# Optimization experiments

Measured on AMD Instinct MI355X. Metric: run time of the kernel, lower is better.

Reference implementation:

```python
import jax, jax.numpy as jnp
import numpy as np
from jax import lax

B, CIN, COUT, K, H, W = 16, 256, 256, 3, 128, 128
R = 16  # LoRA rank


def setup_inputs() -> dict:
    key = jax.random.key(0)
    ks = jax.random.split(key, 16)
    s = 0.05
    return {
        "x": jax.random.normal(ks[0], (B, CIN, H, W), jnp.float32),
        "wms": jax.random.normal(ks[1], (2, B, 32), jnp.float32),
        "conv_w": jax.random.normal(ks[2], (COUT, CIN, K, K), jnp.float32) * s,
        "conv_b": jax.random.normal(ks[3], (COUT,), jnp.float32) * s,
        "e1_w1": jax.random.normal(ks[4], (128, 32), jnp.float32) * s,
        "e1_b1": jax.random.normal(ks[5], (128,), jnp.float32) * s,
        "e1_w2": jax.random.normal(ks[6], (256, 128), jnp.float32) * s,
        "e1_b2": jax.random.normal(ks[7], (256,), jnp.float32) * s,
        "e2_w1": jax.random.normal(ks[8], (128, 32), jnp.float32) * s,
        "e2_b1": jax.random.normal(ks[9], (128,), jnp.float32) * s,
        "e2_w2": jax.random.normal(ks[10], (256, 128), jnp.float32) * s,
        "e2_b2": jax.random.normal(ks[11], (256,), jnp.float32) * s,
        "lora_A1": jax.random.normal(ks[12], (R, CIN * K), jnp.float32),
        "lora_A2": jax.random.normal(ks[13], (R, CIN * K), jnp.float32),
        "lora_B": jax.random.normal(ks[14], (COUT * K, R), jnp.float32) * s,
    }


def _embed(v, w1, b1, w2, b2):
    # Linear(32,128) -> LeakyReLU(0.2) -> Linear(128,256)
    h = v @ w1.T + b1
    h = jnp.where(h >= 0, h, 0.2 * h)
    return h @ w2.T + b2


def _conv_same(x, w):
    # NCHW conv, stride 1, padding 1
    return lax.conv_general_dilated(x, w, (1, 1), [(1, 1), (1, 1)],
                                    dimension_numbers=("NCHW", "OIHW", "NCHW"))


def reference(x, wms, conv_w, conv_b, e1_w1, e1_b1, e1_w2, e1_b2,
              e2_w1, e2_b1, e2_w2, e2_b2, lora_A1, lora_A2, lora_B):
    wm1, wm2 = wms[0], wms[1]
    coff1 = _embed(wm1, e1_w1, e1_b1, e1_w2, e1_b2).reshape(B, R, R)
    coff2 = _embed(wm2, e2_w1, e2_b1, e2_w2, e2_b2).reshape(B, R, R)

    org = _conv_same(x, conv_w) + conv_b[None, :, None, None]

    # per-sample LoRA weights: (COUT*K, R) @ (R,R) @ (R, CIN*K) -> (B, COUT, CIN, K, K)
    wA = jnp.einsum('pr,brq,qc->bpc', lora_B, coff1, lora_A1).reshape(B, COUT, CIN, K, K)
    wB = jnp.einsum('pr,brq,qc->bpc', lora_B, coff2, lora_A2).reshape(B, COUT, CIN, K, K)

    def per_sample_conv(xi, wi):
        return _conv_same(xi[None], wi)[0]

    outA = jax.vmap(per_sample_conv)(x, wA)
    outB = jax.vmap(per_sample_conv)(x, wB)
    return org + outA + outB
```

## Files before the change

### kernel.cpp

```cpp
#include <hip/hip_runtime.h>
#include <hip/hip_bf16.h>
#include <stdint.h>

typedef __bf16 bf16x8 __attribute__((ext_vector_type(8)));
typedef float f32x4 __attribute__((ext_vector_type(4)));
typedef unsigned short ushort8v __attribute__((ext_vector_type(8)));

#define NB    16
#define CIN   256
#define COUT  256
#define HH    128
#define WW    128

#define OFF_ZROW  0u
#define OFF_COFF  (1u << 16)
#define OFF_TMPS  (1u << 17)
#define OFF_WEFF  (1u << 20)
#define OFF_XT    (20u * 1024u * 1024u)
#define XT_PER_B  (128u * 128u * 256u * 2u)

__device__ inline void gload16(const void* g, void* l) {
  __builtin_amdgcn_global_load_lds(
      (const __attribute__((address_space(1))) void*)g,
      (__attribute__((address_space(3))) void*)l, 16, 0, 0);
}

__device__ inline ushort f2bf(float f) {
  __hip_bfloat16 h = __float2bfloat16(f);
  union { __hip_bfloat16 b; ushort u; } cv;
  cv.b = h;
  return cv.u;
}

__global__ void k_coff(const float* __restrict__ wms,
                       const float* __restrict__ w1a, const float* __restrict__ b1a,
                       const float* __restrict__ w2a, const float* __restrict__ b2a,
                       const float* __restrict__ w1b, const float* __restrict__ b1b,
                       const float* __restrict__ w2b, const float* __restrict__ b2b,
                       float* __restrict__ coff) {
  int br = blockIdx.x >> 4, b = blockIdx.x & 15;
  const float* w1 = br ? w1b : w1a;
  const float* b1 = br ? b1b : b1a;
  const float* w2 = br ? w2b : w2a;
  const float* b2 = br ? b2b : b2a;
  const float* v = wms + (br * 16 + b) * 32;
  __shared__ float h[128];
  int t = threadIdx.x;
  if (t < 128) {
    float a = b1[t];
#pragma unroll
    for (int i = 0; i < 32; ++i) a += w1[t * 32 + i] * v[i];
    h[t] = a >= 0.f ? a : 0.2f * a;
  }
  __syncthreads();
  float a = b2[t];
  for (int j = 0; j < 128; ++j) a += w2[t * 128 + j] * h[j];
  coff[(br * 16 + b) * 256 + t] = a;
}

__global__ void k_tmps(const float* __restrict__ coff,
                       const float* __restrict__ A1, const float* __restrict__ A2,
                       float* __restrict__ tmpS) {
  int b = blockIdx.x >> 4, r = blockIdx.x & 15;
  __shared__ float c1[16], c2[16];
  int t = threadIdx.x;
  if (t < 16) {
    c1[t] = coff[b * 256 + r * 16 + t];
    c2[t] = coff[(16 + b) * 256 + r * 16 + t];
  }
  __syncthreads();
  for (int c = t; c < 768; c += 256) {
    float s = 0.f;
#pragma unroll
    for (int q = 0; q < 16; ++q) s += c1[q] * A1[q * 768 + c] + c2[q] * A2[q * 768 + c];
    tmpS[(b * 16 + r) * 768 + c] = s;
  }
}

__global__ __launch_bounds__(256) void k_weff(const float* __restrict__ conv_w,
                                              const float* __restrict__ loraB,
                                              const float* __restrict__ tmpS,
                                              __hip_bfloat16* __restrict__ Weff) {
  int bid = blockIdx.x;
  int co = bid & 255, b = bid >> 8;
  int t = threadIdx.x;
  __shared__ float Bs[3][16];
  __shared__ ushort obuf[2304];
  if (t < 48) Bs[t >> 4][t & 15] = loraB[(co * 3 + (t >> 4)) * 16 + (t & 15)];
  __syncthreads();
  const float* T = tmpS + (size_t)b * 16 * 768;
  const float* W = conv_w + (size_t)co * 2304;
#pragma unroll
  for (int k = 0; k < 3; ++k) {
#pragma unroll
    for (int cc = 0; cc < 3; ++cc) {
      int c = cc * 256 + t;
      float s = W[k * 768 + c];
#pragma unroll
      for (int r = 0; r < 16; ++r) s += Bs[k][r] * T[r * 768 + c];
      int f = k * 768 + c;
      int ci = f / 9, tt = f - ci * 9;
      obuf[tt * 256 + ci] = f2bf(s);
    }
  }
  __syncthreads();
#pragma unroll
  for (int tt = 0; tt < 9; ++tt)
    ((ushort*)Weff)[((size_t)(b * 9 + tt) * 256 + co) * 256 + t] = obuf[tt * 256 + t];
}

__global__ __launch_bounds__(256) void k_xt(const float* __restrict__ x,
                                            __hip_bfloat16* __restrict__ xT, int b0) {
  __shared__ ushort t[32][132];
  int bid = blockIdx.x;
  int cb = bid & 7, h = (bid >> 3) & 127, bp = bid >> 10;
  int b = b0 + bp;
  int tid = threadIdx.x;
  int ci2 = tid >> 5, w4 = (tid & 31) * 4;
  const float* srcb = x + ((size_t)(b * 256 + cb * 32) * 128 + h) * 128;
#pragma unroll
  for (int k = 0; k < 4; ++k) {
    int c = ci2 + k * 8;
    float4 v = *(const float4*)(srcb + (size_t)c * 16384 + w4);
    ushort4 u;
    u.x = f2bf(v.x);
    u.y = f2bf(v.y);
    u.z = f2bf(v.z);
    u.w = f2bf(v.w);
    *(ushort4*)&t[c][w4] = u;
  }
  __syncthreads();
  int w = tid >> 1, hf = tid & 1;
  ushort8v o0, o1;
#pragma unroll
  for (int j = 0; j < 8; ++j) {
    o0[j] = t[hf * 16 + j][w];
    o1[j] = t[hf * 16 + 8 + j][w];
  }
  ushort* dst = (ushort*)xT + (size_t)bp * 128 * 128 * 256 +
                ((size_t)h * 128 + w) * 256 + cb * 32 + hf * 16;
  *(ushort8v*)dst = o0;
  *(ushort8v*)(dst + 8) = o1;
}

__global__ __launch_bounds__(256, 3) void k_conv(
    const __hip_bfloat16* __restrict__ xT,
    const __hip_bfloat16* __restrict__ Weff,
    const __hip_bfloat16* __restrict__ zrow,
    const float* __restrict__ cbias,
    float* __restrict__ out, int b0) {
  __shared__ __align__(16) __hip_bfloat16 xs[3 * 130 * 32];
  __shared__ __align__(16) __hip_bfloat16 wbuf[3 * 128 * 32];

  int nwg = gridDim.x;
  int bid0 = blockIdx.x;
  int bid = (bid0 & 7) * (nwg >> 3) + (bid0 >> 3);

  int h0 = bid & 127, coh = (bid >> 7) & 1, bp = bid >> 8;
  int b = b0 + bp;

  int tid = threadIdx.x;
  int wid = tid >> 6, lane = tid & 63;
  int l15 = lane & 15, lh = lane >> 4;
  int wm = wid >> 1;
  int w0 = (wid & 1) * 64;
  int lrow = lane >> 2;
  int sgx = (lane & 3) ^ (((1 + lrow) >> 1) & 3);
  int sgw = (lane & 3) ^ ((lrow >> 1) & 3);
  int asw = (l15 >> 1) & 3;

  if (tid < 192) {
    int ri = tid >> 6, which = (tid >> 5) & 1, ci = tid & 31;
    ((ushort*)xs)[ri * 4160 + (which ? 129 : 0) * 32 + ci] = 0;
  }

  int a_base = (wm * 64 + l15) * 32 + (lh ^ asw) * 8;
  int b_base0 = (w0 + l15 + 0) * 32 + ((lh ^ (((l15 + 0) >> 1) & 3)) * 8);
  int b_base1 = (w0 + l15 + 1) * 32 + ((lh ^ (((l15 + 1) >> 1) & 3)) * 8);
  int b_base2 = (w0 + l15 + 2) * 32 + ((lh ^ (((l15 + 2) >> 1) & 3)) * 8);
  int xoff = lrow * 256 + sgx * 8;
  int woff = (coh * 128 + lrow) * 256 + sgw * 8;

  const __hip_bfloat16* xTb = xT + (size_t)bp * 128 * 128 * 256;
  const __hip_bfloat16* r0 = (h0 > 0)   ? xTb + (size_t)(h0 - 1) * 32768 : zrow;
  const __hip_bfloat16* r1 = xTb + (size_t)h0 * 32768;
  const __hip_bfloat16* r2 = (h0 < 127) ? xTb + (size_t)(h0 + 1) * 32768 : zrow;

  f32x4 acc[4][4];
#pragma unroll
  for (int mf = 0; mf < 4; ++mf)
#pragma unroll
    for (int nf = 0; nf < 4; ++nf) acc[mf][nf] = (f32x4){0.f, 0.f, 0.f, 0.f};

  for (int cb8 = 0; cb8 < 8; ++cb8) {
    int c0 = cb8 * 32;
    __syncthreads();

#pragma unroll
    for (int k = 0; k < 6; ++k) {
      const int ri = k >> 1;
      int wblk = (k & 1) * 4 + wid;
      const __hip_bfloat16* rp = (ri == 0) ? r0 : ((ri == 1) ? r1 : r2);
      gload16((const void*)(rp + wblk * 4096 + c0 + xoff),
              (void*)(xs + ri * 4160 + (1 + wblk * 16) * 32));
    }

#pragma unroll 1
    for (int kh = 0; kh < 3; ++kh) {
      if (kh) __syncthreads();
      const __hip_bfloat16* wtap =
          Weff + ((size_t)(b * 9 + kh * 3) << 16) + c0 + woff;
#pragma unroll
      for (int k = 0; k < 6; ++k) {
        const int kw = k >> 1;
        int cblk = (k & 1) * 4 + wid;
        gload16((const void*)(wtap + kw * 65536 + cblk * 4096),
                (void*)(wbuf + kw * 4096 + cblk * 512));
      }
      __syncthreads();

#pragma unroll
      for (int kw = 0; kw < 3; ++kw) {
        int bb = (kw == 0) ? b_base0 : ((kw == 1) ? b_base1 : b_base2);
        bf16x8 af[4], bfr[4];
#pragma unroll
        for (int mf = 0; mf < 4; ++mf)
          af[mf] = *(const bf16x8*)&wbuf[kw * 4096 + a_base + mf * 512];
#pragma unroll
        for (int nf = 0; nf < 4; ++nf)
          bfr[nf] = *(const bf16x8*)&xs[kh * 4160 + bb + nf * 512];
#pragma unroll
        for (int mf = 0; mf < 4; ++mf)
#pragma unroll
          for (int nf = 0; nf < 4; ++nf)
            acc[mf][nf] = __builtin_amdgcn_mfma_f32_16x16x32_bf16(af[mf], bfr[nf],
                                                                  acc[mf][nf], 0, 0, 0);
      }
    }
  }

#pragma unroll
  for (int mf = 0; mf < 4; ++mf) {
    int cobase = coh * 128 + wm * 64 + mf * 16 + lh * 4;
#pragma unroll
    for (int r = 0; r < 4; ++r) {
      int co = cobase + r;
      float bias = cbias[co];
      size_t obase = ((size_t)(b * 256 + co) * 128 + h0) * 128 + w0 + l15;
#pragma unroll
      for (int nf = 0; nf < 4; ++nf) out[obase + nf * 16] = acc[mf][nf][r] + bias;
    }
  }
}

extern "C" void kernel_launch(void* const* d_in, const int* in_sizes, int n_in,
                              void* d_out, int out_size, void* d_ws, size_t ws_size,
                              hipStream_t stream) {
  const float* x      = (const float*)d_in[0];
  const float* wms    = (const float*)d_in[1];
  const float* conv_w = (const float*)d_in[2];
  const float* conv_b = (const float*)d_in[3];
  const float* e1w1   = (const float*)d_in[4];
  const float* e1b1   = (const float*)d_in[5];
  const float* e1w2   = (const float*)d_in[6];
  const float* e1b2   = (const float*)d_in[7];
  const float* e2w1   = (const float*)d_in[8];
  const float* e2b1   = (const float*)d_in[9];
  const float* e2w2   = (const float*)d_in[10];
  const float* e2b2   = (const float*)d_in[11];
  const float* A1     = (const float*)d_in[12];
  const float* A2     = (const float*)d_in[13];
  const float* loraB  = (const float*)d_in[14];
  float* out = (float*)d_out;

  uint8_t* ws = (uint8_t*)d_ws;
  __hip_bfloat16* zrow = (__hip_bfloat16*)(ws + OFF_ZROW);
  float* coff          = (float*)(ws + OFF_COFF);
  float* tmpS          = (float*)(ws + OFF_TMPS);
  __hip_bfloat16* Weff = (__hip_bfloat16*)(ws + OFF_WEFF);
  __hip_bfloat16* xT   = (__hip_bfloat16*)(ws + OFF_XT);

  int G = 16;
  while (G > 1 && (size_t)OFF_XT + (size_t)G * XT_PER_B > ws_size) G >>= 1;

  hipMemsetAsync(zrow, 0, 65536, stream);
  k_coff<<<32, 256, 0, stream>>>(wms, e1w1, e1b1, e1w2, e1b2, e2w1, e2b1, e2w2, e2b2, coff);
  k_tmps<<<256, 256, 0, stream>>>(coff, A1, A2, tmpS);
  k_weff<<<16 * 256, 256, 0, stream>>>(conv_w, loraB, tmpS, Weff);
  for (int g = 0; g < 16; g += G) {
    k_xt<<<G * 1024, 256, 0, stream>>>(x, xT, g);
    k_conv<<<G * 256, 256, 0, stream>>>(xT, Weff, zrow, conv_b, out, g);
  }
}
```

Before: 441.1 us.

## Double-buffer weight taps in LDS and software-pipeline fragment reads with MFMA

The per-kh weight staging buffer becomes two LDS slots, so the next kernel row's weights are loaded asynchronously while the current row is computed. This removes one barrier per kh. Within each kh the LDS fragment reads for the next kw are interleaved with the MFMAs of the current kw. In exchange LDS use grows and launch bounds drop from 3 to 2 workgroups per CU, which lowers occupancy and leaves fewer waves to hide latency.

```diff
diff --git a/kernel.cpp b/kernel.cpp
--- a/kernel.cpp
+++ b/kernel.cpp
@@ -143,14 +143,14 @@
   *(ushort8v*)(dst + 8) = o1;
 }
 
-__global__ __launch_bounds__(256, 3) void k_conv(
+__global__ __launch_bounds__(256, 2) void k_conv(
     const __hip_bfloat16* __restrict__ xT,
     const __hip_bfloat16* __restrict__ Weff,
     const __hip_bfloat16* __restrict__ zrow,
     const float* __restrict__ cbias,
     float* __restrict__ out, int b0) {
   __shared__ __align__(16) __hip_bfloat16 xs[3 * 130 * 32];
-  __shared__ __align__(16) __hip_bfloat16 wbuf[3 * 128 * 32];
+  __shared__ __align__(16) __hip_bfloat16 wsl[2 * 3 * 128 * 32];
 
   int nwg = gridDim.x;
   int bid0 = blockIdx.x;
@@ -192,6 +192,54 @@
 #pragma unroll
     for (int nf = 0; nf < 4; ++nf) acc[mf][nf] = (f32x4){0.f, 0.f, 0.f, 0.f};
 
+#define STAGE_W(KH, SLOT)                                                      \
+  {                                                                            \
+    const __hip_bfloat16* wt =                                                 \
+        Weff + ((size_t)(b * 9 + (KH) * 3) << 16) + c0 + woff;                 \
+    _Pragma("unroll")                                                          \
+    for (int k = 0; k < 6; ++k) {                                              \
+      const int kw = k >> 1;                                                   \
+      int cblk = (k & 1) * 4 + wid;                                            \
+      gload16((const void*)(wt + kw * 65536 + cblk * 4096),                    \
+              (void*)(wsl + (SLOT) * 12288 + kw * 4096 + cblk * 512));         \
+    }                                                                          \
+  }
+
+#define READF(KH, SLOT, KW, AF, BF)                                            \
+  {                                                                            \
+    _Pragma("unroll")                                                          \
+    for (int mf = 0; mf < 4; ++mf)                                             \
+      AF[mf] = *(const bf16x8*)&wsl[(SLOT) * 12288 + (KW) * 4096 + a_base +    \
+                                    mf * 512];                                 \
+    const int bb =                                                             \
+        ((KW) == 0) ? b_base0 : (((KW) == 1) ? b_base1 : b_base2);             \
+    _Pragma("unroll")                                                          \
+    for (int nf = 0; nf < 4; ++nf)                                             \
+      BF[nf] = *(const bf16x8*)&xs[(KH) * 4160 + bb + nf * 512];               \
+  }
+
+#define MF16(AF, BF)                                                           \
+  {                                                                            \
+    _Pragma("unroll")                                                          \
+    for (int mf = 0; mf < 4; ++mf)                                             \
+      _Pragma("unroll")                                                        \
+      for (int nf = 0; nf < 4; ++nf)                                           \
+        acc[mf][nf] = __builtin_amdgcn_mfma_f32_16x16x32_bf16(                 \
+            AF[mf], BF[nf], acc[mf][nf], 0, 0, 0);                             \
+  }
+
+#define COMPUTE_KH(KH, SLOT)                                                   \
+  {                                                                            \
+    bf16x8 afA[4], bfA[4], afB[4], bfB[4];                                     \
+    READF(KH, SLOT, 0, afA, bfA);                                              \
+    READF(KH, SLOT, 1, afB, bfB);                                              \
+    MF16(afA, bfA);                                                            \
+    READF(KH, SLOT, 2, afA, bfA);                                              \
+    MF16(afB, bfB);                                                            \
+    MF16(afA, bfA);                                                            \
+  }
+
+#pragma unroll 1
   for (int cb8 = 0; cb8 < 8; ++cb8) {
     int c0 = cb8 * 32;
     __syncthreads();
@@ -204,40 +252,23 @@
       gload16((const void*)(rp + wblk * 4096 + c0 + xoff),
               (void*)(xs + ri * 4160 + (1 + wblk * 16) * 32));
     }
-
-#pragma unroll 1
-    for (int kh = 0; kh < 3; ++kh) {
-      if (kh) __syncthreads();
-      const __hip_bfloat16* wtap =
-          Weff + ((size_t)(b * 9 + kh * 3) << 16) + c0 + woff;
-#pragma unroll
-      for (int k = 0; k < 6; ++k) {
-        const int kw = k >> 1;
-        int cblk = (k & 1) * 4 + wid;
-        gload16((const void*)(wtap + kw * 65536 + cblk * 4096),
-                (void*)(wbuf + kw * 4096 + cblk * 512));
-      }
-      __syncthreads();
-
-#pragma unroll
-      for (int kw = 0; kw < 3; ++kw) {
-        int bb = (kw == 0) ? b_base0 : ((kw == 1) ? b_base1 : b_base2);
-        bf16x8 af[4], bfr[4];
-#pragma unroll
-        for (int mf = 0; mf < 4; ++mf)
-          af[mf] = *(const bf16x8*)&wbuf[kw * 4096 + a_base + mf * 512];
-#pragma unroll
-        for (int nf = 0; nf < 4; ++nf)
-          bfr[nf] = *(const bf16x8*)&xs[kh * 4160 + bb + nf * 512];
-#pragma unroll
-        for (int mf = 0; mf < 4; ++mf)
-#pragma unroll
-          for (int nf = 0; nf < 4; ++nf)
-            acc[mf][nf] = __builtin_amdgcn_mfma_f32_16x16x32_bf16(af[mf], bfr[nf],
-                                                                  acc[mf][nf], 0, 0, 0);
-      }
-    }
-  }
+    STAGE_W(0, 0);
+    __syncthreads();
+
+    STAGE_W(1, 1);
+    COMPUTE_KH(0, 0);
+    __syncthreads();
+
+    STAGE_W(2, 0);
+    COMPUTE_KH(1, 1);
+    __syncthreads();
+
+    COMPUTE_KH(2, 0);
+  }
+#undef STAGE_W
+#undef READF
+#undef MF16
+#undef COMPUTE_KH
 
 #pragma unroll
   for (int mf = 0; mf < 4; ++mf) {
```

New measurement: 465.1 us. 5.4% more time.

## Load conv weights directly to registers and double-buffer input tile in LDS

Applied to the files above, without the earlier changes.

The weight operand is no longer staged through shared memory. Each wave now loads its A fragments straight from global memory into registers, with two register sets ping-ponged across the kh taps. The input row tile is double-buffered in LDS so the next channel block is prefetched during compute, cutting barriers from several per channel block to one. The cost is much higher register pressure (24 bf16x8 A fragments), with launch bounds lowered to 2 waves per SIMD, and uncoalesced-ish global loads for weights that rely on L2 reuse.

```diff
diff --git a/kernel.cpp b/kernel.cpp
--- a/kernel.cpp
+++ b/kernel.cpp
@@ -143,14 +143,13 @@
   *(ushort8v*)(dst + 8) = o1;
 }
 
-__global__ __launch_bounds__(256, 3) void k_conv(
+__global__ __launch_bounds__(256, 2) void k_conv(
     const __hip_bfloat16* __restrict__ xT,
     const __hip_bfloat16* __restrict__ Weff,
     const __hip_bfloat16* __restrict__ zrow,
     const float* __restrict__ cbias,
     float* __restrict__ out, int b0) {
-  __shared__ __align__(16) __hip_bfloat16 xs[3 * 130 * 32];
-  __shared__ __align__(16) __hip_bfloat16 wbuf[3 * 128 * 32];
+  __shared__ __align__(16) __hip_bfloat16 xs[2 * 3 * 130 * 32];
 
   int nwg = gridDim.x;
   int bid0 = blockIdx.x;
@@ -166,25 +165,25 @@
   int w0 = (wid & 1) * 64;
   int lrow = lane >> 2;
   int sgx = (lane & 3) ^ (((1 + lrow) >> 1) & 3);
-  int sgw = (lane & 3) ^ ((lrow >> 1) & 3);
-  int asw = (l15 >> 1) & 3;
-
-  if (tid < 192) {
-    int ri = tid >> 6, which = (tid >> 5) & 1, ci = tid & 31;
-    ((ushort*)xs)[ri * 4160 + (which ? 129 : 0) * 32 + ci] = 0;
-  }
-
-  int a_base = (wm * 64 + l15) * 32 + (lh ^ asw) * 8;
+
+#pragma unroll
+  for (int bufi = 0; bufi < 2; ++bufi)
+    if (tid < 192) {
+      int ri = tid >> 6, which = (tid >> 5) & 1, ci = tid & 31;
+      ((ushort*)xs)[bufi * 12480 + ri * 4160 + (which ? 129 : 0) * 32 + ci] = 0;
+    }
+
   int b_base0 = (w0 + l15 + 0) * 32 + ((lh ^ (((l15 + 0) >> 1) & 3)) * 8);
   int b_base1 = (w0 + l15 + 1) * 32 + ((lh ^ (((l15 + 1) >> 1) & 3)) * 8);
   int b_base2 = (w0 + l15 + 2) * 32 + ((lh ^ (((l15 + 2) >> 1) & 3)) * 8);
   int xoff = lrow * 256 + sgx * 8;
-  int woff = (coh * 128 + lrow) * 256 + sgw * 8;
 
   const __hip_bfloat16* xTb = xT + (size_t)bp * 128 * 128 * 256;
   const __hip_bfloat16* r0 = (h0 > 0)   ? xTb + (size_t)(h0 - 1) * 32768 : zrow;
   const __hip_bfloat16* r1 = xTb + (size_t)h0 * 32768;
   const __hip_bfloat16* r2 = (h0 < 127) ? xTb + (size_t)(h0 + 1) * 32768 : zrow;
+  const __hip_bfloat16* wAb =
+      Weff + ((size_t)(b * 9) << 16) + (coh * 128 + wm * 64 + l15) * 256 + lh * 8;
 
   f32x4 acc[4][4];
 #pragma unroll
@@ -192,52 +191,72 @@
 #pragma unroll
     for (int nf = 0; nf < 4; ++nf) acc[mf][nf] = (f32x4){0.f, 0.f, 0.f, 0.f};
 
-  for (int cb8 = 0; cb8 < 8; ++cb8) {
-    int c0 = cb8 * 32;
+#define LOAD_A(DST, KH)                                                        \
+  {                                                                            \
+    const __hip_bfloat16* wt = wAb + (((size_t)(KH) * 3) << 16) + c0;          \
+    _Pragma("unroll")                                                          \
+    for (int kw = 0; kw < 3; ++kw)                                             \
+      _Pragma("unroll")                                                        \
+      for (int mf = 0; mf < 4; ++mf)                                           \
+        DST[kw * 4 + mf] = *(const bf16x8*)(wt + kw * 65536 + mf * 4096);      \
+  }
+
+#define COMPUTE_KH(KH, AR)                                                     \
+  {                                                                            \
+    _Pragma("unroll")                                                          \
+    for (int kw = 0; kw < 3; ++kw) {                                           \
+      const int bb = (kw == 0) ? b_base0 : ((kw == 1) ? b_base1 : b_base2);    \
+      bf16x8 bfr[4];                                                           \
+      _Pragma("unroll")                                                        \
+      for (int nf = 0; nf < 4; ++nf)                                           \
+        bfr[nf] = *(const bf16x8*)&xsb[(KH) * 4160 + bb + nf * 512];           \
+      _Pragma("unroll")                                                        \
+      for (int mf = 0; mf < 4; ++mf)                                           \
+        _Pragma("unroll")                                                      \
+        for (int nf = 0; nf < 4; ++nf)                                         \
+          acc[mf][nf] = __builtin_amdgcn_mfma_f32_16x16x32_bf16(               \
+              AR[kw * 4 + mf], bfr[nf], acc[mf][nf], 0, 0, 0);                 \
+    }                                                                          \
+  }
+
+#define STAGE_X(CN)                                                            \
+  {                                                                            \
+    __hip_bfloat16* xd = xs + ((CN) & 1) * 12480;                              \
+    int cs = (CN) * 32;                                                        \
+    _Pragma("unroll")                                                          \
+    for (int k = 0; k < 6; ++k) {                                              \
+      const int ri = k >> 1;                                                   \
+      int wblk = (k & 1) * 4 + wid;                                            \
+      const __hip_bfloat16* rp = (ri == 0) ? r0 : ((ri == 1) ? r1 : r2);       \
+      gload16((const void*)(rp + wblk * 4096 + cs + xoff),                     \
+              (void*)(xd + ri * 4160 + (1 + wblk * 16) * 32));                 \
+    }                                                                          \
+  }
+
+  STAGE_X(0);
+  __syncthreads();
+
+  bf16x8 aA[12], aB[12];
+
+#pragma unroll 1
+  for (int c = 0; c < 8; ++c) {
+    const __hip_bfloat16* xsb = xs + (c & 1) * 12480;
+    int c0 = c * 32;
+
+    LOAD_A(aA, 0);
+    LOAD_A(aB, 1);
+    if (c < 7) STAGE_X(c + 1);
+
+    COMPUTE_KH(0, aA);
+    LOAD_A(aA, 2);
+    COMPUTE_KH(1, aB);
+    COMPUTE_KH(2, aA);
+
     __syncthreads();
-
-#pragma unroll
-    for (int k = 0; k < 6; ++k) {
-      const int ri = k >> 1;
-      int wblk = (k & 1) * 4 + wid;
-      const __hip_bfloat16* rp = (ri == 0) ? r0 : ((ri == 1) ? r1 : r2);
-      gload16((const void*)(rp + wblk * 4096 + c0 + xoff),
-              (void*)(xs + ri * 4160 + (1 + wblk * 16) * 32));
-    }
-
-#pragma unroll 1
-    for (int kh = 0; kh < 3; ++kh) {
-      if (kh) __syncthreads();
-      const __hip_bfloat16* wtap =
-          Weff + ((size_t)(b * 9 + kh * 3) << 16) + c0 + woff;
-#pragma unroll
-      for (int k = 0; k < 6; ++k) {
-        const int kw = k >> 1;
-        int cblk = (k & 1) * 4 + wid;
-        gload16((const void*)(wtap + kw * 65536 + cblk * 4096),
-                (void*)(wbuf + kw * 4096 + cblk * 512));
-      }
-      __syncthreads();
-
-#pragma unroll
-      for (int kw = 0; kw < 3; ++kw) {
-        int bb = (kw == 0) ? b_base0 : ((kw == 1) ? b_base1 : b_base2);
-        bf16x8 af[4], bfr[4];
-#pragma unroll
-        for (int mf = 0; mf < 4; ++mf)
-          af[mf] = *(const bf16x8*)&wbuf[kw * 4096 + a_base + mf * 512];
-#pragma unroll
-        for (int nf = 0; nf < 4; ++nf)
-          bfr[nf] = *(const bf16x8*)&xs[kh * 4160 + bb + nf * 512];
-#pragma unroll
-        for (int mf = 0; mf < 4; ++mf)
-#pragma unroll
-          for (int nf = 0; nf < 4; ++nf)
-            acc[mf][nf] = __builtin_amdgcn_mfma_f32_16x16x32_bf16(af[mf], bfr[nf],
-                                                                  acc[mf][nf], 0, 0, 0);
-      }
-    }
-  }
+  }
+#undef LOAD_A
+#undef COMPUTE_KH
+#undef STAGE_X
 
 #pragma unroll
   for (int mf = 0; mf < 4; ++mf) {
```

New measurement: 724.9 us. 64.3% more time.
